# Kernel tuning notes

Measured on AMD Instinct MI355X. Metric: run time of the kernel, lower is better.

The kernel has to match this reference:

```python
import jax, jax.numpy as jnp
import numpy as np

NUM_HEADS = 6
KS = 3  # kernel_size


def _offset_vectors():
    # torch: arange(-s//2+1, s//2+1) with s=3 -> [-1, 0, 1]; meshgrid 'ij'; stack last; reshape(27,3)
    r = jnp.arange(-(KS // 2), KS // 2 + 1, dtype=jnp.float32)
    gi, gj, gt = jnp.meshgrid(r, r, r, indexing='ij')
    return jnp.stack([gi, gj, gt], -1).reshape(KS ** 3, 3)  # [27, 3]


def setup_inputs() -> dict:
    key = jax.random.key(0)
    kq, kk, kr = jax.random.split(key, 3)
    B, H, W, T, C = 1, 64, 64, 64, 96
    q = jax.random.normal(kq, (B, H, W, T, C), dtype=jnp.float32)
    k = jax.random.normal(kk, (B, H, W, T, C), dtype=jnp.float32)
    rpb = jax.random.normal(kr, (NUM_HEADS, KS, KS, KS), dtype=jnp.float32) * 0.02
    return {"q": q, "k": k, "rpb": rpb}


def reference(q, k, rpb):
    B, H, W, T, C = q.shape
    nh, hd = NUM_HEADS, C // NUM_HEADS
    scale = hd ** (-0.5)
    pdr = (KS - 1) // 2

    qh = q.reshape(B, H, W, T, nh, hd) * scale           # [B,H,W,T,nh,hd]
    kh = k.reshape(B, H, W, T, nh, hd)
    kp = jnp.pad(kh, ((0, 0), (pdr, pdr), (pdr, pdr), (pdr, pdr), (0, 0), (0, 0)))

    # Neighborhood attention logits: dot(q, k_neighbor) + rpb  -> [B,H,W,T,nh,KS^3]
    logits = []
    for di in range(KS):
        for dj in range(KS):
            for dt in range(KS):
                kw = kp[:, di:di + H, dj:dj + W, dt:dt + T]   # shifted window
                a = jnp.einsum('bhwtnc,bhwtnc->bhwtn', qh, kw) + rpb[:, di, dj, dt]
                logits.append(a)
    attn = jnp.stack(logits, -1)                         # [B,H,W,T,nh,27]
    attn = jax.nn.softmax(attn, axis=-1)

    v = _offset_vectors()                                 # [27, 3]
    x = attn @ v                                          # [B,H,W,T,nh,3]
    # -> [B, nh, 3, H, W, T] -> [B, nh*3, H, W, T]
    x = jnp.transpose(x, (0, 4, 5, 1, 2, 3)).reshape(B, nh * 3, H, W, T)
    return x
```

## Files before the change

### kernel.cpp

```cpp
#include <hip/hip_runtime.h>


#define DH 64
#define DW 64
#define DT 64
#define DC 96
#define NH 6
#define HD 16

__device__ __forceinline__ float quad_reduce_add(float x) {
    int i = __float_as_int(x);
    i = __builtin_amdgcn_mov_dpp(i, 0xB1, 0xF, 0xF, true);
    x += __int_as_float(i);
    i = __float_as_int(x);
    i = __builtin_amdgcn_mov_dpp(i, 0x4E, 0xF, 0xF, true);
    x += __int_as_float(i);
    return x;
}

__global__ __launch_bounds__(384) void natten3d_kernel(
    const float* __restrict__ q,
    const float* __restrict__ k,
    const float* __restrict__ rpb,
    float* __restrict__ out)
{
    int bid = blockIdx.x;
    int nb  = (bid & 7) * 512 + (bid >> 3);
    int h = nb >> 6;
    int w = nb & 63;

    int tid  = threadIdx.x;
    int s    = tid & 3;
    int r    = tid >> 2;
    int n    = r % NH;
    int t0   = (r / NH) * 4;
    int tout = t0 + s;

    float4 qv[4];
    {
        const float* qp = q + ((size_t)((h * DW + w) * DT + t0)) * DC + n * HD + s * 4;
        #pragma unroll
        for (int u = 0; u < 4; ++u) {
            float4 v = *reinterpret_cast<const float4*>(qp + u * DC);
            v.x *= 0.25f; v.y *= 0.25f; v.z *= 0.25f; v.w *= 0.25f;
            qv[u] = v;
        }
    }

    int  coff[9];
    bool cok[9];
    #pragma unroll
    for (int c = 0; c < 9; ++c) {
        int di = c / 3, dj = c % 3;
        int hh = h + di - 1, ww = w + dj - 1;
        cok[c] = ((unsigned)hh < DH) && ((unsigned)ww < DW);
        int hc = min(max(hh, 0), DH - 1);
        int wc = min(max(ww, 0), DW - 1);
        coff[c] = (hc * DW + wc) * DT * DC;
    }

    int soff[6];
    #pragma unroll
    for (int j = 0; j < 6; ++j) {
        int tt = min(max(t0 + j - 1, 0), DT - 1);
        soff[j] = tt * DC + n * HD + s * 4;
    }

    float acc_l = 0.f, acc0 = 0.f, acc1 = 0.f, acc2 = 0.f;
    const int rbase = n * 27;

    #pragma unroll
    for (int c = 0; c < 9; ++c) {
        const int di = c / 3, dj = c % 3;

        float4 kb[6];
        #pragma unroll
        for (int j = 0; j < 6; ++j)
            kb[j] = *reinterpret_cast<const float4*>(k + (size_t)(coff[c] + soff[j]));

        float rb0 = rpb[rbase + c * 3 + 0];
        float rb1 = rpb[rbase + c * 3 + 1];
        float rb2 = rpb[rbase + c * 3 + 2];

        float kd0 = 0.f, kd1 = 0.f, kd2 = 0.f;
        #pragma unroll
        for (int u = 0; u < 4; ++u) {
            #pragma unroll
            for (int d = 0; d < 3; ++d) {
                const int j = u + d;
                float p = qv[u].x * kb[j].x;
                p = fmaf(qv[u].y, kb[j].y, p);
                p = fmaf(qv[u].z, kb[j].z, p);
                p = fmaf(qv[u].w, kb[j].w, p);
                float dot = quad_reduce_add(p);
                const bool mine = (s == u);
                if (d == 0)      kd0 = mine ? dot : kd0;
                else if (d == 1) kd1 = mine ? dot : kd1;
                else             kd2 = mine ? dot : kd2;
            }
        }

        #pragma unroll
        for (int d = 0; d < 3; ++d) {
            float dot = (d == 0) ? kd0 : (d == 1) ? kd1 : kd2;
            bool valid = cok[c] && ((unsigned)(tout + d - 1) < DT);
            float logit = (valid ? dot : 0.f) + ((d == 0) ? rb0 : (d == 1) ? rb1 : rb2);
            float p = __expf(logit);
            acc_l += p;
            if (di == 0) acc0 -= p; else if (di == 2) acc0 += p;
            if (dj == 0) acc1 -= p; else if (dj == 2) acc1 += p;
            if (d  == 0) acc2 -= p; else if (d  == 2) acc2 += p;
        }
    }

    float inv = 1.f / acc_l;
    size_t plane = (size_t)DH * DW * DT;
    size_t sp = (size_t)((h * DW + w) * DT) + tout;
    out[(size_t)(n * 3 + 0) * plane + sp] = acc0 * inv;
    out[(size_t)(n * 3 + 1) * plane + sp] = acc1 * inv;
    out[(size_t)(n * 3 + 2) * plane + sp] = acc2 * inv;
}

extern "C" void kernel_launch(void* const* d_in, const int* in_sizes, int n_in,
                              void* d_out, int out_size, void* d_ws, size_t ws_size,
                              hipStream_t stream) {
    const float* q   = (const float*)d_in[0];
    const float* k   = (const float*)d_in[1];
    const float* rpb = (const float*)d_in[2];
    float* out = (float*)d_out;

    dim3 grid(DH * DW);
    dim3 block(16 * NH * 4);
    hipLaunchKernelGGL(natten3d_kernel, grid, block, 0, stream, q, k, rpb, out);
}
```

Before: 271.3 us.

## Double-buffer K loads and use transpose-reduce instead of per-dot quad reductions

Replaces twelve full quad reductions per neighbor column with a butterfly transpose-reduce: each lane selects partial sums so that three DPP adds leave each lane with its own dot, instead of two DPP ops per partial with select-masking. K loads are double-buffered across the nine (di,dj) columns, so the next column's loads are issued before the current one is computed. Also sets launch bounds min blocks to 4, which may constrain registers while the extra buffer increases register pressure.

```diff
diff --git a/kernel.cpp b/kernel.cpp
--- a/kernel.cpp
+++ b/kernel.cpp
@@ -8,17 +8,14 @@
 #define NH 6
 #define HD 16
 
-__device__ __forceinline__ float quad_reduce_add(float x) {
-    int i = __float_as_int(x);
-    i = __builtin_amdgcn_mov_dpp(i, 0xB1, 0xF, 0xF, true);
-    x += __int_as_float(i);
-    i = __float_as_int(x);
-    i = __builtin_amdgcn_mov_dpp(i, 0x4E, 0xF, 0xF, true);
-    x += __int_as_float(i);
-    return x;
+__device__ __forceinline__ float dpp_xor1(float x) {
+    return __int_as_float(__builtin_amdgcn_mov_dpp(__float_as_int(x), 0xB1, 0xF, 0xF, true));
+}
+__device__ __forceinline__ float dpp_xor2(float x) {
+    return __int_as_float(__builtin_amdgcn_mov_dpp(__float_as_int(x), 0x4E, 0xF, 0xF, true));
 }
 
-__global__ __launch_bounds__(384) void natten3d_kernel(
+__global__ __launch_bounds__(384, 4) void natten3d_kernel(
     const float* __restrict__ q,
     const float* __restrict__ k,
     const float* __restrict__ rpb,
@@ -35,6 +32,11 @@
     int n    = r % NH;
     int t0   = (r / NH) * 4;
     int tout = t0 + s;
+
+    const bool m1 = (s & 1) != 0;
+    const bool m2 = (s & 2) != 0;
+    const bool dok0 = (tout >= 1);
+    const bool dok2 = (tout <= DT - 2);
 
     float4 qv[4];
     {
@@ -69,49 +71,65 @@
     float acc_l = 0.f, acc0 = 0.f, acc1 = 0.f, acc2 = 0.f;
     const int rbase = n * 27;
 
-    #pragma unroll
-    for (int c = 0; c < 9; ++c) {
-        const int di = c / 3, dj = c % 3;
+    float4 kbA[6], kbB[6];
+    float  rbA[3], rbB[3];
 
-        float4 kb[6];
-        #pragma unroll
-        for (int j = 0; j < 6; ++j)
-            kb[j] = *reinterpret_cast<const float4*>(k + (size_t)(coff[c] + soff[j]));
+#define ISSUE(c, kb, rb) do {                                                  \
+    const float* kc_ = k + (size_t)coff[c];                                    \
+    _Pragma("unroll")                                                          \
+    for (int j = 0; j < 6; ++j)                                                \
+        kb[j] = *reinterpret_cast<const float4*>(kc_ + soff[j]);               \
+    rb[0] = rpb[rbase + (c) * 3 + 0];                                          \
+    rb[1] = rpb[rbase + (c) * 3 + 1];                                          \
+    rb[2] = rpb[rbase + (c) * 3 + 2];                                          \
+} while (0)
 
-        float rb0 = rpb[rbase + c * 3 + 0];
-        float rb1 = rpb[rbase + c * 3 + 1];
-        float rb2 = rpb[rbase + c * 3 + 2];
+#define COMPUTE(c, kb, rb) do {                                                \
+    _Pragma("unroll")                                                          \
+    for (int d = 0; d < 3; ++d) {                                              \
+                         \
+        float p0_ = kb[d+0].x*qv[0].x; p0_ = fmaf(qv[0].y,kb[d+0].y,p0_);      \
+        p0_ = fmaf(qv[0].z,kb[d+0].z,p0_); p0_ = fmaf(qv[0].w,kb[d+0].w,p0_);  \
+        float p1_ = kb[d+1].x*qv[1].x; p1_ = fmaf(qv[1].y,kb[d+1].y,p1_);      \
+        p1_ = fmaf(qv[1].z,kb[d+1].z,p1_); p1_ = fmaf(qv[1].w,kb[d+1].w,p1_);  \
+        float p2_ = kb[d+2].x*qv[2].x; p2_ = fmaf(qv[2].y,kb[d+2].y,p2_);      \
+        p2_ = fmaf(qv[2].z,kb[d+2].z,p2_); p2_ = fmaf(qv[2].w,kb[d+2].w,p2_);  \
+        float p3_ = kb[d+3].x*qv[3].x; p3_ = fmaf(qv[3].y,kb[d+3].y,p3_);      \
+        p3_ = fmaf(qv[3].z,kb[d+3].z,p3_); p3_ = fmaf(qv[3].w,kb[d+3].w,p3_);  \
+                \
+        float u1_ = m1 ? p1_ : p0_;                                            \
+        float v1_ = m1 ? p0_ : p1_;                                            \
+        u1_ += dpp_xor1(v1_);                                                  \
+        float w1_ = m1 ? p3_ : p2_;                                            \
+        float x1_ = m1 ? p2_ : p3_;                                            \
+        w1_ += dpp_xor1(x1_);                                                  \
+        float u2_ = m2 ? w1_ : u1_;                                            \
+        float v2_ = m2 ? u1_ : w1_;                                            \
+        float dot_ = u2_ + dpp_xor2(v2_);                                      \
+        bool valid_ = cok[c] && (d == 0 ? dok0 : (d == 2 ? dok2 : true));      \
+        float logit_ = (valid_ ? dot_ : 0.f) + rb[d];  \
+        float pe_ = __expf(logit_);            \
+        acc_l += pe_;                                                          \
+        if ((c)/3 == 0) acc0 -= pe_; else if ((c)/3 == 2) acc0 += pe_;         \
+        if ((c)%3 == 0) acc1 -= pe_; else if ((c)%3 == 2) acc1 += pe_;         \
+        if (d == 0)     acc2 -= pe_; else if (d == 2)     acc2 += pe_;         \
+    }                                                                          \
+} while (0)
 
-        float kd0 = 0.f, kd1 = 0.f, kd2 = 0.f;
-        #pragma unroll
-        for (int u = 0; u < 4; ++u) {
-            #pragma unroll
-            for (int d = 0; d < 3; ++d) {
-                const int j = u + d;
-                float p = qv[u].x * kb[j].x;
-                p = fmaf(qv[u].y, kb[j].y, p);
-                p = fmaf(qv[u].z, kb[j].z, p);
-                p = fmaf(qv[u].w, kb[j].w, p);
-                float dot = quad_reduce_add(p);
-                const bool mine = (s == u);
-                if (d == 0)      kd0 = mine ? dot : kd0;
-                else if (d == 1) kd1 = mine ? dot : kd1;
-                else             kd2 = mine ? dot : kd2;
-            }
-        }
+    ISSUE(0, kbA, rbA);
+    ISSUE(1, kbB, rbB);
+    COMPUTE(0, kbA, rbA); ISSUE(2, kbA, rbA);
+    COMPUTE(1, kbB, rbB); ISSUE(3, kbB, rbB);
+    COMPUTE(2, kbA, rbA); ISSUE(4, kbA, rbA);
+    COMPUTE(3, kbB, rbB); ISSUE(5, kbB, rbB);
+    COMPUTE(4, kbA, rbA); ISSUE(6, kbA, rbA);
+    COMPUTE(5, kbB, rbB); ISSUE(7, kbB, rbB);
+    COMPUTE(6, kbA, rbA); ISSUE(8, kbA, rbA);
+    COMPUTE(7, kbB, rbB);
+    COMPUTE(8, kbA, rbA);
 
-        #pragma unroll
-        for (int d = 0; d < 3; ++d) {
-            float dot = (d == 0) ? kd0 : (d == 1) ? kd1 : kd2;
-            bool valid = cok[c] && ((unsigned)(tout + d - 1) < DT);
-            float logit = (valid ? dot : 0.f) + ((d == 0) ? rb0 : (d == 1) ? rb1 : rb2);
-            float p = __expf(logit);
-            acc_l += p;
-            if (di == 0) acc0 -= p; else if (di == 2) acc0 += p;
-            if (dj == 0) acc1 -= p; else if (dj == 2) acc1 += p;
-            if (d  == 0) acc2 -= p; else if (d  == 2) acc2 += p;
-        }
-    }
+#undef ISSUE
+#undef COMPUTE
 
     float inv = 1.f / acc_l;
     size_t plane = (size_t)DH * DW * DT;
```

Measured after the change: 279.3 us. 1.03x slower.

## Use butterfly transpose-reduce for quad dot products and halve block size

Applied to the files above, without the earlier changes.

The per-lane quad reduction (two DPP swaps for each of 12 dot products per window column) becomes a butterfly exchange. Each lane selects partner values so that three DPP moves produce the specific dot product that lane owns, which cuts the DPP and select work. The launch is also split so each block covers half of the T range with 192 threads, doubling the grid. That gives finer scheduling granularity but repeats the per-block setup of offsets, masks and rpb loads.

```diff
diff --git a/kernel.cpp b/kernel.cpp
--- a/kernel.cpp
+++ b/kernel.cpp
@@ -8,33 +8,37 @@
 #define NH 6
 #define HD 16
 
-__device__ __forceinline__ float quad_reduce_add(float x) {
-    int i = __float_as_int(x);
-    i = __builtin_amdgcn_mov_dpp(i, 0xB1, 0xF, 0xF, true);
-    x += __int_as_float(i);
-    i = __float_as_int(x);
-    i = __builtin_amdgcn_mov_dpp(i, 0x4E, 0xF, 0xF, true);
-    x += __int_as_float(i);
-    return x;
+__device__ __forceinline__ float dpp_xor1(float x) {
+    return __int_as_float(__builtin_amdgcn_mov_dpp(__float_as_int(x), 0xB1, 0xF, 0xF, true));
+}
+__device__ __forceinline__ float dpp_xor2(float x) {
+    return __int_as_float(__builtin_amdgcn_mov_dpp(__float_as_int(x), 0x4E, 0xF, 0xF, true));
 }
 
-__global__ __launch_bounds__(384) void natten3d_kernel(
+__global__ __launch_bounds__(192) void natten3d_kernel(
     const float* __restrict__ q,
     const float* __restrict__ k,
     const float* __restrict__ rpb,
     float* __restrict__ out)
 {
     int bid = blockIdx.x;
-    int nb  = (bid & 7) * 512 + (bid >> 3);
-    int h = nb >> 6;
-    int w = nb & 63;
+    int nb  = (bid & 7) * 1024 + (bid >> 3);
+    int thalf = nb & 1;
+    int w     = (nb >> 1) & 63;
+    int h     = nb >> 7;
 
-    int tid  = threadIdx.x;
-    int s    = tid & 3;
-    int r    = tid >> 2;
-    int n    = r % NH;
-    int t0   = (r / NH) * 4;
-    int tout = t0 + s;
+    int tid   = threadIdx.x;
+    int s     = tid & 3;
+    int r     = tid >> 2;
+    int n     = r % NH;
+    int strip = r / NH;
+    int t0    = thalf * 32 + strip * 4;
+    int tout  = t0 + s;
+
+    const bool m1 = (s & 1) != 0;
+    const bool m2 = (s & 2) != 0;
+    const bool dok0 = (tout >= 1);
+    const bool dok2 = (tout <= DT - 2);
 
     float4 qv[4];
     {
@@ -71,8 +75,6 @@
 
     #pragma unroll
     for (int c = 0; c < 9; ++c) {
-        const int di = c / 3, dj = c % 3;
-
         float4 kb[6];
         #pragma unroll
         for (int j = 0; j < 6; ++j)
@@ -82,34 +84,35 @@
         float rb1 = rpb[rbase + c * 3 + 1];
         float rb2 = rpb[rbase + c * 3 + 2];
 
-        float kd0 = 0.f, kd1 = 0.f, kd2 = 0.f;
-        #pragma unroll
-        for (int u = 0; u < 4; ++u) {
-            #pragma unroll
-            for (int d = 0; d < 3; ++d) {
-                const int j = u + d;
-                float p = qv[u].x * kb[j].x;
-                p = fmaf(qv[u].y, kb[j].y, p);
-                p = fmaf(qv[u].z, kb[j].z, p);
-                p = fmaf(qv[u].w, kb[j].w, p);
-                float dot = quad_reduce_add(p);
-                const bool mine = (s == u);
-                if (d == 0)      kd0 = mine ? dot : kd0;
-                else if (d == 1) kd1 = mine ? dot : kd1;
-                else             kd2 = mine ? dot : kd2;
-            }
-        }
-
         #pragma unroll
         for (int d = 0; d < 3; ++d) {
-            float dot = (d == 0) ? kd0 : (d == 1) ? kd1 : kd2;
-            bool valid = cok[c] && ((unsigned)(tout + d - 1) < DT);
-            float logit = (valid ? dot : 0.f) + ((d == 0) ? rb0 : (d == 1) ? rb1 : rb2);
-            float p = __expf(logit);
-            acc_l += p;
-            if (di == 0) acc0 -= p; else if (di == 2) acc0 += p;
-            if (dj == 0) acc1 -= p; else if (dj == 2) acc1 += p;
-            if (d  == 0) acc2 -= p; else if (d  == 2) acc2 += p;
+            float p0 = kb[d+0].x * qv[0].x; p0 = fmaf(qv[0].y, kb[d+0].y, p0);
+            p0 = fmaf(qv[0].z, kb[d+0].z, p0); p0 = fmaf(qv[0].w, kb[d+0].w, p0);
+            float p1 = kb[d+1].x * qv[1].x; p1 = fmaf(qv[1].y, kb[d+1].y, p1);
+            p1 = fmaf(qv[1].z, kb[d+1].z, p1); p1 = fmaf(qv[1].w, kb[d+1].w, p1);
+            float p2 = kb[d+2].x * qv[2].x; p2 = fmaf(qv[2].y, kb[d+2].y, p2);
+            p2 = fmaf(qv[2].z, kb[d+2].z, p2); p2 = fmaf(qv[2].w, kb[d+2].w, p2);
+            float p3 = kb[d+3].x * qv[3].x; p3 = fmaf(qv[3].y, kb[d+3].y, p3);
+            p3 = fmaf(qv[3].z, kb[d+3].z, p3); p3 = fmaf(qv[3].w, kb[d+3].w, p3);
+
+            float u1 = m1 ? p1 : p0;
+            float v1 = m1 ? p0 : p1;
+            u1 += dpp_xor1(v1);
+            float w1 = m1 ? p3 : p2;
+            float x1 = m1 ? p2 : p3;
+            w1 += dpp_xor1(x1);
+            float u2 = m2 ? w1 : u1;
+            float v2 = m2 ? u1 : w1;
+            float dot = u2 + dpp_xor2(v2);
+
+            bool valid = cok[c] && (d == 0 ? dok0 : (d == 2 ? dok2 : true));
+            float rb = (d == 0) ? rb0 : (d == 1) ? rb1 : rb2;
+            float logit = (valid ? dot : 0.f) + rb;
+            float pe = __expf(logit);
+            acc_l += pe;
+            if (c / 3 == 0) acc0 -= pe; else if (c / 3 == 2) acc0 += pe;
+            if (c % 3 == 0) acc1 -= pe; else if (c % 3 == 2) acc1 += pe;
+            if (d == 0)     acc2 -= pe; else if (d == 2)     acc2 += pe;
         }
     }
 
@@ -129,7 +132,7 @@
     const float* rpb = (const float*)d_in[2];
     float* out = (float*)d_out;
 
-    dim3 grid(DH * DW);
-    dim3 block(16 * NH * 4);
+    dim3 grid(DH * DW * 2);
+    dim3 block(8 * NH * 4);
     hipLaunchKernelGGL(natten3d_kernel, grid, block, 0, stream, q, k, rpb, out);
 }
```

After: 262.3 us. 3.3% less time.
